# Kernel optimization log

Hardware: AMD Instinct MI355X
Metric: run time of the kernel (lower is better)

Reference implementation:

```python
import jax, jax.numpy as jnp
import numpy as np

N_SIN = 3  # fcn_n_sin

def _feats(x):
    # x: [B, Din] -> features [B, Din, 1 + 2*N_SIN]
    omega = (2.0 ** jnp.arange(N_SIN, dtype=x.dtype))  # [n_sin]
    ox = x[..., None] * omega  # [B, Din, n_sin]
    return jnp.concatenate([x[..., None], jnp.sin(ox), jnp.cos(ox)], axis=-1)

def setup_inputs() -> dict:
    key = jax.random.key(0)
    k1, k2, k3 = jax.random.split(key, 3)
    B, Din, Dout, H, F = 2048, 64, 64, 32, 1 + 2 * N_SIN
    x = jax.random.normal(k1, (B, Din), dtype=jnp.float32)
    # xavier-normal-ish init for W1/W2, zeros for biases (matches init_parameters)
    W1 = jax.random.normal(k2, (Din, Dout, H, F), dtype=jnp.float32) * np.sqrt(2.0 / (H + F))
    W2 = jax.random.normal(k3, (Din, Dout, 1, H), dtype=jnp.float32) * np.sqrt(2.0 / (1 + H))
    B1 = jnp.zeros((Din, Dout, H), dtype=jnp.float32)
    B2 = jnp.zeros((Din, Dout, 1), dtype=jnp.float32)
    return {"x": x, "W1": W1, "W2": W2, "B1": B1, "B2": B2}

def reference(x, W1, W2, B1, B2):
    f = _feats(x)  # [B, Din, F]
    # per-edge first layer: [B, Din, Dout, H]
    h = jnp.einsum('bif,iohf->bioh', f, W1) + B1[None]
    h = jax.nn.silu(h)
    # per-edge second layer -> scalar: [B, Din, Dout]
    phis = jnp.einsum('bioh,ioh->bio', h, W2[:, :, 0, :]) + B2[:, :, 0][None]
    return phis.sum(axis=1)  # [B, Dout]
```

## Files before the change

### kernel.cpp

```cpp
#include <hip/hip_runtime.h>
#include <math.h>

typedef _Float16 f16;
typedef f16   f16x4    __attribute__((ext_vector_type(4)));
typedef f16   f16x8    __attribute__((ext_vector_type(8)));
typedef float floatx2  __attribute__((ext_vector_type(2)));
typedef float floatx4  __attribute__((ext_vector_type(4)));
typedef float floatx16 __attribute__((ext_vector_type(16)));

#define LOG2E   1.44269504088896340736f
#define INV_2PI 0.15915494309189533577f

#define B_SZ  2048
#define DIN   64
#define DOUT  64
#define NH    32

#define NIG   4
#define IGW   (DIN / NIG)

#define W1IMG_ELEMS ((size_t)DIN * DOUT * 64 * 4)
#define FIMG_ELEMS  ((size_t)DIN * 64 * 64 * 4)

__device__ __forceinline__ floatx2 pk_add(floatx2 a, floatx2 b) {
    floatx2 d; asm("v_pk_add_f32 %0, %1, %2" : "=v"(d) : "v"(a), "v"(b)); return d;
}
__device__ __forceinline__ floatx2 pk_mul(floatx2 a, floatx2 b) {
    floatx2 d; asm("v_pk_mul_f32 %0, %1, %2" : "=v"(d) : "v"(a), "v"(b)); return d;
}
__device__ __forceinline__ floatx2 pk_fma(floatx2 a, floatx2 b, floatx2 c) {
    floatx2 d; asm("v_pk_fma_f32 %0, %1, %2, %3" : "=v"(d) : "v"(a), "v"(b), "v"(c)); return d;
}

__global__ __launch_bounds__(256) void prep_kernel(
        const float* __restrict__ W1, const float* __restrict__ B1,
        const float* __restrict__ W2, const float* __restrict__ B2,
        const float* __restrict__ x,
        f16* __restrict__ w1img, f16* __restrict__ w12img,
        f16* __restrict__ fimg, float* __restrict__ b2sum,
        float* __restrict__ out) {
    const int bid = blockIdx.x, tid = threadIdx.x;
    if (bid < 1024) {
        const bool second = bid >= 512;
        int u = (second ? bid - 512 : bid) * 256 + tid;
        int lane2 = u & 31, o = (u >> 5) & 63, i = u >> 11;
        int l0 = lane2 * 2;
        f16x8 v;
        if (lane2 < 16) {
#pragma unroll
            for (int t = 0; t < 2; ++t) {
                int m = l0 + t;
                float sc = -LOG2E;
                if (second) sc *= W2[(size_t)(i * 64 + o) * 32 + m];
                const float* w = W1 + (size_t)((i * 64 + o) * 32 + m) * 7;
#pragma unroll
                for (int j = 0; j < 4; ++j) v[t * 4 + j] = (f16)(w[j] * sc);
            }
        } else {
#pragma unroll
            for (int t = 0; t < 2; ++t) {
                int m = l0 - 32 + t;
                float sc = -LOG2E;
                if (second) sc *= W2[(size_t)(i * 64 + o) * 32 + m];
                const float* w = W1 + (size_t)((i * 64 + o) * 32 + m) * 7;
                v[t * 4 + 0] = (f16)(w[4] * sc);
                v[t * 4 + 1] = (f16)(w[5] * sc);
                v[t * 4 + 2] = (f16)(w[6] * sc);
                v[t * 4 + 3] = (f16)(B1[(i * 64 + o) * 32 + m] * sc);
            }
        }
        *(f16x8*)((second ? w12img : w1img) + (size_t)u * 8) = v;
    } else if (bid < 1536) {
        int u = (bid - 1024) * 256 + tid;
        int lane2 = u & 31, btp = (u >> 5) & 63, i = u >> 11;
        int l0 = lane2 * 2;
        f16x8 v;
#pragma unroll
        for (int t = 0; t < 2; ++t) {
            int b = btp * 32 + ((l0 + t) & 31);
            float xv = x[b * 64 + i];
            float s1 = __builtin_amdgcn_sinf(xv * INV_2PI);
            float c1 = __builtin_amdgcn_cosf(xv * INV_2PI);
            float s2 = 2.0f * s1 * c1, c2 = 1.0f - 2.0f * s1 * s1;
            float s4 = 2.0f * s2 * c2, c4 = 1.0f - 2.0f * s2 * s2;
            if (lane2 < 16) { v[t*4+0] = (f16)xv; v[t*4+1] = (f16)s1;
                              v[t*4+2] = (f16)s2; v[t*4+3] = (f16)s4; }
            else            { v[t*4+0] = (f16)c1; v[t*4+1] = (f16)c2;
                              v[t*4+2] = (f16)c4; v[t*4+3] = (f16)1.0f; }
        }
        *(f16x8*)(fimg + (size_t)u * 8) = v;
    } else if (bid < 1664) {
        int t = (bid - 1536) * 256 + tid;
        floatx4 z = {};
        *(floatx4*)(out + (size_t)t * 4) = z;
    } else if (tid < 64) {
        float s = 0.0f;
        for (int i = 0; i < 64; ++i) s += B2[i * 64 + tid];
        b2sum[tid] = s;
    }
}

__device__ __forceinline__ void silu8(
        floatx2 A0, floatx2 A1, floatx2 A2, floatx2 A3,
        floatx2 U0, floatx2 U1, floatx2 U2, floatx2 U3,
        floatx2 one2, float& phi) {
    floatx2 E0 = {__builtin_amdgcn_exp2f(A0[0]), __builtin_amdgcn_exp2f(A0[1])};
    floatx2 E1 = {__builtin_amdgcn_exp2f(A1[0]), __builtin_amdgcn_exp2f(A1[1])};
    floatx2 E2 = {__builtin_amdgcn_exp2f(A2[0]), __builtin_amdgcn_exp2f(A2[1])};
    floatx2 E3 = {__builtin_amdgcn_exp2f(A3[0]), __builtin_amdgcn_exp2f(A3[1])};
    floatx2 D0 = pk_add(E0, one2), D1 = pk_add(E1, one2);
    floatx2 D2 = pk_add(E2, one2), D3 = pk_add(E3, one2);
    floatx2 N01 = pk_fma(U0, D1, pk_mul(U1, D0));
    floatx2 N23 = pk_fma(U2, D3, pk_mul(U3, D2));
    floatx2 P01 = pk_mul(D0, D1), P23 = pk_mul(D2, D3);
    floatx2 N   = pk_fma(N01, P23, pk_mul(N23, P01));
    floatx2 DD  = pk_mul(P01, P23);
    float n8 = __builtin_fmaf(N[0], DD[1], N[1] * DD[0]);
    float d8 = DD[0] * DD[1];
    phi = __builtin_fmaf(n8, __builtin_amdgcn_rcpf(d8), phi);
}

__global__ __launch_bounds__(128, 6) void main_kernel(
        const f16* __restrict__ w1img, const f16* __restrict__ w12img,
        const f16* __restrict__ fimg, const float* __restrict__ b2sum,
        float* __restrict__ out) {
    const int tid  = threadIdx.x;
    const int lane = tid & 63;
    const int wv   = tid >> 6;
    const int btp  = blockIdx.x & 63;
    const int og   = (blockIdx.x >> 6) & 31;
    const int ig   = blockIdx.x >> 11;
    const int o    = __builtin_amdgcn_readfirstlane(og * 2 + wv);
    const size_t ibase = (size_t)ig * IGW;

    const f16* ap1 = w1img  + ibase * 16384 + ((size_t)o   * 64 + lane) * 4;
    const f16* ap2 = w12img + ibase * 16384 + ((size_t)o   * 64 + lane) * 4;
    const f16* bp  = fimg   + ibase * 16384 + ((size_t)btp * 64 + lane) * 4;

    const floatx16 zeroC = {};
    const floatx2  one2  = {1.0f, 1.0f};
    float phiL = 0.0f, phiH = 0.0f;

    f16x4 fa1 = *(const f16x4*)ap1;
    f16x4 fa2 = *(const f16x4*)ap2;
    f16x4 fb  = *(const f16x4*)bp;

#pragma unroll 1
    for (int ii = 0; ii < IGW; ++ii) {
        floatx16 C1 = __builtin_amdgcn_mfma_f32_32x32x8f16(fa1, fb, zeroC, 0, 0, 0);
        floatx16 C2 = __builtin_amdgcn_mfma_f32_32x32x8f16(fa2, fb, zeroC, 0, 0, 0);

        const size_t i1 = (size_t)(ii + 1);
        fa1 = *(const f16x4*)(ap1 + i1 * 16384);
        fa2 = *(const f16x4*)(ap2 + i1 * 16384);
        fb  = *(const f16x4*)(bp  + i1 * 16384);

        silu8((floatx2){C1[0],  C1[1]},  (floatx2){C1[4],  C1[5]},
              (floatx2){C1[8],  C1[9]},  (floatx2){C1[12], C1[13]},
              (floatx2){C2[0],  C2[1]},  (floatx2){C2[4],  C2[5]},
              (floatx2){C2[8],  C2[9]},  (floatx2){C2[12], C2[13]},
              one2, phiL);
        silu8((floatx2){C1[2],  C1[3]},  (floatx2){C1[6],  C1[7]},
              (floatx2){C1[10], C1[11]}, (floatx2){C1[14], C1[15]},
              (floatx2){C2[2],  C2[3]},  (floatx2){C2[6],  C2[7]},
              (floatx2){C2[10], C2[11]}, (floatx2){C2[14], C2[15]},
              one2, phiH);
    }

    float phi = phiL + phiH;
    phi += __shfl_xor(phi, 32, 64);

    if (lane < 32) {
        float v = phi * (-1.0f / LOG2E) + (1.0f / NIG) * b2sum[o];
        unsafeAtomicAdd(out + (size_t)(btp * 32 + lane) * 64 + o, v);
    }
}

extern "C" void kernel_launch(void* const* d_in, const int* in_sizes, int n_in,
                              void* d_out, int out_size, void* d_ws, size_t ws_size,
                              hipStream_t stream) {
    const float* x  = (const float*)d_in[0];
    const float* W1 = (const float*)d_in[1];
    const float* W2 = (const float*)d_in[2];
    const float* B1 = (const float*)d_in[3];
    const float* B2 = (const float*)d_in[4];
    float* out = (float*)d_out;

    f16*   w1img  = (f16*)d_ws;
    f16*   w12img = w1img  + W1IMG_ELEMS;
    f16*   fimg   = w12img + W1IMG_ELEMS;
    float* b2sum  = (float*)(fimg + FIMG_ELEMS);

    prep_kernel<<<1665, 256, 0, stream>>>(W1, B1, W2, B2, x,
                                          w1img, w12img, fimg, b2sum, out);
    main_kernel<<<NIG * 32 * 64, 128, 0, stream>>>(w1img, w12img, fimg, b2sum, out);
}
```

Measured before the change: 111.4 us.

## Software-pipeline MFMA one step ahead, merge SiLU reductions, halve input-groups

The main loop now issues the next iteration's first MFMA before running the current SiLU, so the matrix unit overlaps the transcendental work. The two 8-wide rational SiLU reductions are merged into one 16-wide reduction that needs a single reciprocal. The input dimension is split into 2 groups instead of 4, giving fewer blocks and atomics but longer loops, and the occupancy hint drops from 6 to 4 waves. Side effects: more register pressure, reads past the group end by two steps, and a wider product of denominators that could overflow in fp32.

```diff
diff --git a/kernel.cpp b/kernel.cpp
--- a/kernel.cpp
+++ b/kernel.cpp
@@ -14,9 +14,9 @@
 #define B_SZ  2048
 #define DIN   64
 #define DOUT  64
-#define NH    32
-
-#define NIG   4
+#define N_HID 32
+
+#define NIG   2
 #define IGW   (DIN / NIG)
 
 #define W1IMG_ELEMS ((size_t)DIN * DOUT * 64 * 4)
@@ -100,27 +100,44 @@
     }
 }
 
-__device__ __forceinline__ void silu8(
-        floatx2 A0, floatx2 A1, floatx2 A2, floatx2 A3,
-        floatx2 U0, floatx2 U1, floatx2 U2, floatx2 U3,
-        floatx2 one2, float& phi) {
-    floatx2 E0 = {__builtin_amdgcn_exp2f(A0[0]), __builtin_amdgcn_exp2f(A0[1])};
-    floatx2 E1 = {__builtin_amdgcn_exp2f(A1[0]), __builtin_amdgcn_exp2f(A1[1])};
-    floatx2 E2 = {__builtin_amdgcn_exp2f(A2[0]), __builtin_amdgcn_exp2f(A2[1])};
-    floatx2 E3 = {__builtin_amdgcn_exp2f(A3[0]), __builtin_amdgcn_exp2f(A3[1])};
+__device__ __forceinline__ void silu16(
+        const floatx16& C1, const floatx16& C2, floatx2 one2, float& phi) {
+    floatx2 E0 = {__builtin_amdgcn_exp2f(C1[0]),  __builtin_amdgcn_exp2f(C1[1])};
+    floatx2 E1 = {__builtin_amdgcn_exp2f(C1[4]),  __builtin_amdgcn_exp2f(C1[5])};
+    floatx2 E2 = {__builtin_amdgcn_exp2f(C1[8]),  __builtin_amdgcn_exp2f(C1[9])};
+    floatx2 E3 = {__builtin_amdgcn_exp2f(C1[12]), __builtin_amdgcn_exp2f(C1[13])};
+    floatx2 F0 = {__builtin_amdgcn_exp2f(C1[2]),  __builtin_amdgcn_exp2f(C1[3])};
+    floatx2 F1 = {__builtin_amdgcn_exp2f(C1[6]),  __builtin_amdgcn_exp2f(C1[7])};
+    floatx2 F2 = {__builtin_amdgcn_exp2f(C1[10]), __builtin_amdgcn_exp2f(C1[11])};
+    floatx2 F3 = {__builtin_amdgcn_exp2f(C1[14]), __builtin_amdgcn_exp2f(C1[15])};
     floatx2 D0 = pk_add(E0, one2), D1 = pk_add(E1, one2);
     floatx2 D2 = pk_add(E2, one2), D3 = pk_add(E3, one2);
-    floatx2 N01 = pk_fma(U0, D1, pk_mul(U1, D0));
-    floatx2 N23 = pk_fma(U2, D3, pk_mul(U3, D2));
-    floatx2 P01 = pk_mul(D0, D1), P23 = pk_mul(D2, D3);
-    floatx2 N   = pk_fma(N01, P23, pk_mul(N23, P01));
-    floatx2 DD  = pk_mul(P01, P23);
-    float n8 = __builtin_fmaf(N[0], DD[1], N[1] * DD[0]);
-    float d8 = DD[0] * DD[1];
-    phi = __builtin_fmaf(n8, __builtin_amdgcn_rcpf(d8), phi);
-}
-
-__global__ __launch_bounds__(128, 6) void main_kernel(
+    floatx2 G0 = pk_add(F0, one2), G1 = pk_add(F1, one2);
+    floatx2 G2 = pk_add(F2, one2), G3 = pk_add(F3, one2);
+    floatx2 U0 = {C2[0], C2[1]},   U1 = {C2[4], C2[5]};
+    floatx2 U2 = {C2[8], C2[9]},   U3 = {C2[12], C2[13]};
+    floatx2 V0 = {C2[2], C2[3]},   V1 = {C2[6], C2[7]};
+    floatx2 V2 = {C2[10], C2[11]}, V3 = {C2[14], C2[15]};
+    floatx2 nLo01 = pk_fma(U0, D1, pk_mul(U1, D0));
+    floatx2 nLo23 = pk_fma(U2, D3, pk_mul(U3, D2));
+    floatx2 pLo01 = pk_mul(D0, D1), pLo23 = pk_mul(D2, D3);
+    floatx2 nLo   = pk_fma(nLo01, pLo23, pk_mul(nLo23, pLo01));
+    floatx2 dLo   = pk_mul(pLo01, pLo23);
+    floatx2 nHi01 = pk_fma(V0, G1, pk_mul(V1, G0));
+    floatx2 nHi23 = pk_fma(V2, G3, pk_mul(V3, G2));
+    floatx2 pHi01 = pk_mul(G0, G1), pHi23 = pk_mul(G2, G3);
+    floatx2 nHi   = pk_fma(nHi01, pHi23, pk_mul(nHi23, pHi01));
+    floatx2 dHi   = pk_mul(pHi01, pHi23);
+    float n8L = __builtin_fmaf(nLo[0], dLo[1], nLo[1] * dLo[0]);
+    float d8L = dLo[0] * dLo[1];
+    float n8H = __builtin_fmaf(nHi[0], dHi[1], nHi[1] * dHi[0]);
+    float d8H = dHi[0] * dHi[1];
+    float n16 = __builtin_fmaf(n8L, d8H, n8H * d8L);
+    float d16 = d8L * d8H;
+    phi = __builtin_fmaf(n16, __builtin_amdgcn_rcpf(d16), phi);
+}
+
+__global__ __launch_bounds__(128, 4) void main_kernel(
         const f16* __restrict__ w1img, const f16* __restrict__ w12img,
         const f16* __restrict__ fimg, const float* __restrict__ b2sum,
         float* __restrict__ out) {
@@ -139,35 +156,31 @@
 
     const floatx16 zeroC = {};
     const floatx2  one2  = {1.0f, 1.0f};
-    float phiL = 0.0f, phiH = 0.0f;
-
-    f16x4 fa1 = *(const f16x4*)ap1;
-    f16x4 fa2 = *(const f16x4*)ap2;
-    f16x4 fb  = *(const f16x4*)bp;
+    float phi = 0.0f;
+
+    f16x4 fa1c = *(const f16x4*)ap1;
+    f16x4 fa2c = *(const f16x4*)ap2;
+    f16x4 fbc  = *(const f16x4*)bp;
+    floatx16 C1c = __builtin_amdgcn_mfma_f32_32x32x8f16(fa1c, fbc, zeroC, 0, 0, 0);
+    f16x4 fa1n = *(const f16x4*)(ap1 + 16384);
+    f16x4 fa2n = *(const f16x4*)(ap2 + 16384);
+    f16x4 fbn  = *(const f16x4*)(bp  + 16384);
 
 #pragma unroll 1
     for (int ii = 0; ii < IGW; ++ii) {
-        floatx16 C1 = __builtin_amdgcn_mfma_f32_32x32x8f16(fa1, fb, zeroC, 0, 0, 0);
-        floatx16 C2 = __builtin_amdgcn_mfma_f32_32x32x8f16(fa2, fb, zeroC, 0, 0, 0);
-
-        const size_t i1 = (size_t)(ii + 1);
-        fa1 = *(const f16x4*)(ap1 + i1 * 16384);
-        fa2 = *(const f16x4*)(ap2 + i1 * 16384);
-        fb  = *(const f16x4*)(bp  + i1 * 16384);
-
-        silu8((floatx2){C1[0],  C1[1]},  (floatx2){C1[4],  C1[5]},
-              (floatx2){C1[8],  C1[9]},  (floatx2){C1[12], C1[13]},
-              (floatx2){C2[0],  C2[1]},  (floatx2){C2[4],  C2[5]},
-              (floatx2){C2[8],  C2[9]},  (floatx2){C2[12], C2[13]},
-              one2, phiL);
-        silu8((floatx2){C1[2],  C1[3]},  (floatx2){C1[6],  C1[7]},
-              (floatx2){C1[10], C1[11]}, (floatx2){C1[14], C1[15]},
-              (floatx2){C2[2],  C2[3]},  (floatx2){C2[6],  C2[7]},
-              (floatx2){C2[10], C2[11]}, (floatx2){C2[14], C2[15]},
-              one2, phiH);
+        floatx16 C2c = __builtin_amdgcn_mfma_f32_32x32x8f16(fa2c, fbc, zeroC, 0, 0, 0);
+        floatx16 C1n = __builtin_amdgcn_mfma_f32_32x32x8f16(fa1n, fbn, zeroC, 0, 0, 0);
+        fa2c = fa2n; fbc = fbn;
+        const size_t i2 = (size_t)(ii + 2);
+        fa1n = *(const f16x4*)(ap1 + i2 * 16384);
+        fa2n = *(const f16x4*)(ap2 + i2 * 16384);
+        fbn  = *(const f16x4*)(bp  + i2 * 16384);
+
+        silu16(C1c, C2c, one2, phi);
+
+        C1c = C1n;
     }
 
-    float phi = phiL + phiH;
     phi += __shfl_xor(phi, 32, 64);
 
     if (lane < 32) {
```

Result: slower. 116.9 us (+4.9%).
